# Performance work log

Hardware: AMD Instinct MI355X
Metric: run time of the kernel (lower is better)

Reference implementation:

```python
import jax, jax.numpy as jnp
import numpy as np

# ---- straight-through estimators (match torch floor_ste/round_ste in I-ViT) ----
def ste_floor(x):
    return x + jax.lax.stop_gradient(jnp.floor(x) - x)

def ste_round(x):
    return x + jax.lax.stop_gradient(jnp.round(x) - x)

# ---- QuantAct: symmetric per-tensor activation quantization ----
def quant_act(x, bit):
    qmax = 2.0 ** (bit - 1) - 1
    s = jnp.max(jnp.abs(jax.lax.stop_gradient(x))) / qmax
    x_int = jnp.clip(ste_round(x / s), -qmax - 1.0, qmax)
    return x_int * s, s

# ---- QuantLinear: per-output-channel symmetric weight quant, integer GEMM ----
def quant_linear(x, s_x, W, b=None, bit=8):
    qmax = 2.0 ** (bit - 1) - 1
    w_s = jnp.max(jnp.abs(jax.lax.stop_gradient(W)), axis=1, keepdims=True) / qmax  # [out,1]
    W_int = jnp.clip(ste_round(W / w_s), -qmax - 1.0, qmax)
    x_int = x / s_x                                   # [B,N,in] integer-valued
    out_s = w_s[:, 0] * s_x                           # [out] per-channel scale
    out_int = jnp.einsum('bni,oi->bno', x_int, W_int)
    if b is not None:
        out_int = out_int + ste_round(b / out_s)
    return out_int * out_s, out_s

# ---- IntSoftmax (I-ViT shift-based integer exp, output_bit=16) ----
def int_softmax(x, s, output_bit=16, n=15):
    x_int = x / s
    x_int = x_int - jnp.max(x_int, axis=-1, keepdims=True)
    # int_exp_shift: x*log2(e) approx via x + x/2 - x/16
    x_int = x_int + ste_floor(x_int / 2.0) - ste_floor(x_int / 16.0)
    x0 = jnp.floor(-1.0 / jax.lax.stop_gradient(s))   # floor(-1/s), negative
    x_int = jnp.maximum(x_int, n * x0)
    q = ste_floor(x_int / x0)                         # in [0, n]
    r = x_int - x0 * q
    exp_int = r / 2.0 - x0
    exp_int = jnp.clip(ste_floor(exp_int * jnp.exp2(n - q)), 0.0, None)
    exp_sum = jnp.minimum(jnp.sum(exp_int, axis=-1, keepdims=True), 2.0 ** 31 - 1)
    factor = ste_floor((2.0 ** 31 - 1) / exp_sum)
    exp_int = ste_floor(exp_int * factor / 2.0 ** (31 - output_bit + 1))
    out_s = jnp.asarray(1.0 / 2.0 ** (output_bit - 1), x.dtype)
    return exp_int * out_s, out_s

NUM_HEADS = 12

def attention_forward(x, s_in, W_qkv, W_proj, b_proj):
    B, N, C = x.shape
    H = NUM_HEADS
    D = C // H
    scale = D ** -0.5
    s_in = s_in.reshape(())
    # qkv QuantLinear (no bias) -> QuantAct(8)
    h, _ = quant_linear(x, s_in, W_qkv, None)
    h, s1 = quant_act(h, 8)
    qkv = h.reshape(B, N, 3, H, D).transpose(2, 0, 3, 1, 4)  # [3,B,H,N,D]
    q, k, v = qkv[0], qkv[1], qkv[2]
    # QuantMatMul 1: integer q @ k^T, rescale
    attn = jnp.einsum('bhnd,bhmd->bhnm', q / s1, k / s1) * (s1 * s1)
    s_attn = s1 * s1
    attn = attn * scale
    s_attn = s_attn * scale
    attn, s_attn = quant_act(attn, 8)
    attn, s_sm = int_softmax(attn, s_attn, output_bit=16)
    # QuantMatMul 2: integer attn @ v, rescale
    out = jnp.einsum('bhnm,bhmd->bhnd', attn / s_sm, v / s1) * (s_sm * s1)
    out = out.transpose(0, 2, 1, 3).reshape(B, N, C)
    out, s_o = quant_act(out, 8)
    out, _ = quant_linear(out, s_o, W_proj, b_proj)
    out, s_out = quant_act(out, 16)
    return out, s_out

def setup_inputs() -> dict:
    key = jax.random.key(0)
    k1, k2, k3, k4 = jax.random.split(key, 4)
    B, N, C = 8, 784, 768
    x = jax.random.normal(k1, (B, N, C), dtype=jnp.float32)
    # pre-quantize x so it is an integer multiple of its scaling factor (8-bit)
    s = jnp.max(jnp.abs(x)) / 127.0
    x = jnp.round(x / s) * s
    W_qkv = jax.random.normal(k2, (3 * C, C), dtype=jnp.float32) * (C ** -0.5)
    W_proj = jax.random.normal(k3, (C, C), dtype=jnp.float32) * (C ** -0.5)
    b_proj = jax.random.normal(k4, (C,), dtype=jnp.float32) * 0.02
    return {"x": x, "act_scaling_factor": s.reshape(1), "W_qkv": W_qkv,
            "W_proj": W_proj, "b_proj": b_proj}

def reference(x, act_scaling_factor, W_qkv, W_proj, b_proj):
    return attention_forward(x, act_scaling_factor, W_qkv, W_proj, b_proj)
```

## Files before the change

### kernel.cpp

```cpp
#include <hip/hip_runtime.h>
#include <cstdint>
#include <cstddef>

#define DEV __device__ __forceinline__

namespace {

constexpr int kN = 784, kC = 768, kH = 12, kD = 64;
constexpr int kM = 6272, kOC = 2304, kBH = 96;
constexpr int kNp = 832;
constexpr size_t SZ_QKV1 = (size_t)kBH * kN * kD;
constexpr size_t SZ_VT   = (size_t)kBH * kD * kNp;
constexpr double kEps   = 2.0e-3;
constexpr double kEpsW  = 3.0e-5;
constexpr double kEpsX0 = 3.0e-5;
constexpr long long kDS = 1024;
constexpr long long kEP = 128;
constexpr double kGuard = 1.0e-9;

using i32x4 = __attribute__((ext_vector_type(4))) int;

DEV void mfma_i8_acc(i32x4& c, i32x4 a, i32x4 b) {
  c = __builtin_amdgcn_mfma_i32_16x16x64_i8(a, b, c, 0, 0, 0);
}

DEV double wave_max_d(double v) {
  for (int o = 32; o; o >>= 1) v = fmax(v, __shfl_xor(v, o));
  return v;
}
DEV int wave_max_i(int v) {
  for (int o = 32; o; o >>= 1) v = max(v, __shfl_xor(v, o));
  return v;
}

DEV double ctl_hmax(const char* c)  { return __longlong_as_double(*(const long long*)(c)); }
DEV int    ctl_qkmax(const char* c) { return *(const int*)(c + 8); }
DEV double ctl_pmax(const char* c)  { return __longlong_as_double(*(const long long*)(c + 16)); }
DEV double ctl_pvmax(const char* c) { return __longlong_as_double(*(const long long*)(c + 24)); }

DEV double get_s1(const char* c) { return ctl_hmax(c) / 127.0; }
DEV double get_sa(const char* c) {
  double s1 = get_s1(c);
  double amax = ((double)ctl_qkmax(c) * (s1 * s1)) * 0.125;
  return amax / 127.0;
}
DEV double get_c2(const char* c) { return get_s1(c) * 3.0517578125e-05; }
DEV double get_so(const char* c) { return (ctl_pvmax(c) * get_c2(c)) / 127.0; }

DEV int p_eval(int xi, int x0i) {
  int x2 = xi + (xi >> 1) - (xi >> 4);
  x2 = max(x2, 15 * x0i);
  int q = x2 / x0i;
  int rrem = x2 - x0i * q;
  int base = rrem - 2 * x0i;
  return (q <= 14) ? (base << (14 - q)) : (base >> 1);
}

DEV int p4_final(long long p, long long fLo, long long fHi) {
  long long a = (p * fLo - kEP) >> 16;
  long long b = (p * fLo + kEP) >> 16;
  if (fLo == fHi) return (int)((a + b) << 1);
  long long c = (p * fHi - kEP) >> 16;
  long long d = (p * fHi + kEP) >> 16;
  return (int)(a + b + c + d);
}

__global__ __launch_bounds__(256) void k_quant_w(
    const float* __restrict__ Wq, const float* __restrict__ Wp,
    const float* __restrict__ s_in_p,
    int8_t* __restrict__ wq8A, int8_t* __restrict__ wq8B,
    int8_t* __restrict__ wp8A, int8_t* __restrict__ wp8B,
    double* __restrict__ outs_q, double* __restrict__ wsp) {
  int r = blockIdx.x;
  bool isq = r < kOC;
  const float* row = isq ? Wq + (size_t)r * kC : Wp + (size_t)(r - kOC) * kC;
  double m = 0.0;
  for (int i = threadIdx.x; i < kC; i += 256) m = fmax(m, fabs((double)row[i]));
  m = wave_max_d(m);
  __shared__ double sred[4];
  __shared__ double s_ws;
  if ((threadIdx.x & 63) == 0) sred[threadIdx.x >> 6] = m;
  __syncthreads();
  if (threadIdx.x == 0) {
    double mm = fmax(fmax(sred[0], sred[1]), fmax(sred[2], sred[3]));
    double ws = mm / 127.0;
    s_ws = ws;
    if (isq) outs_q[r] = ws * (double)s_in_p[0];
    else     wsp[r - kOC] = ws;
  }
  __syncthreads();
  double ws = s_ws;
  int8_t* dA = isq ? wq8A + (size_t)r * kC : wp8A + (size_t)(r - kOC) * kC;
  int8_t* dB = isq ? wq8B + (size_t)r * kC : wp8B + (size_t)(r - kOC) * kC;
  for (int i = threadIdx.x; i < kC; i += 256) {
    double arg = (double)row[i] / ws;
    dA[i] = (int8_t)(int)fmin(fmax(rint(arg - kEpsW), -128.0), 127.0);
    dB[i] = (int8_t)(int)fmin(fmax(rint(arg + kEpsW), -128.0), 127.0);
  }
}

__global__ __launch_bounds__(256) void k_quant_x(
    const float* __restrict__ x, const float* __restrict__ s_in_p,
    int8_t* __restrict__ x8) {
  double s = (double)s_in_p[0];
  int total = kM * kC;
  for (int i = blockIdx.x * 256 + threadIdx.x; i < total; i += gridDim.x * 256)
    x8[i] = (int8_t)(int)rint((double)x[i] / s);
}

template <int MODE>
__global__ __launch_bounds__(256) void k_gemm1m(
    const int8_t* __restrict__ A, const int8_t* __restrict__ Bm,
    const double* __restrict__ outs_q, char* __restrict__ ctl,
    int8_t* __restrict__ qkv8, int8_t* __restrict__ vT8, double dit) {
  __shared__ __align__(16) int8_t As[128][80];
  __shared__ __align__(16) int8_t Bs[128][80];
  int bm = blockIdx.y * 128, bn = blockIdx.x * 128;
  int tid = threadIdx.x;
  int w = tid >> 6, l = tid & 63;
  int frow = l & 15, fk = (l >> 4) << 4;
  int rb = w * 32;
  i32x4 acc[2][8];
#pragma unroll
  for (int i = 0; i < 2; ++i)
#pragma unroll
    for (int s = 0; s < 8; ++s) { acc[i][s][0]=0; acc[i][s][1]=0; acc[i][s][2]=0; acc[i][s][3]=0; }
  for (int k0 = 0; k0 < kC; k0 += 64) {
    __syncthreads();
#pragma unroll
    for (int e = 0; e < 2; ++e) {
      int idx = tid + e * 256;
      int row = idx >> 2, cg = (idx & 3) << 4;
      *(int4*)&As[row][cg] = *(const int4*)&A[(size_t)(bm + row) * kC + k0 + cg];
      *(int4*)&Bs[row][cg] = *(const int4*)&Bm[(size_t)(bn + row) * kC + k0 + cg];
    }
    __syncthreads();
    i32x4 af0 = *(const i32x4*)&As[rb + frow][fk];
    i32x4 af1 = *(const i32x4*)&As[rb + 16 + frow][fk];
#pragma unroll
    for (int s = 0; s < 8; ++s) {
      i32x4 bf = *(const i32x4*)&Bs[s * 16 + frow][fk];
      mfma_i8_acc(acc[0][s], af0, bf);
      mfma_i8_acc(acc[1][s], af1, bf);
    }
  }
  if (MODE == 0) {
    double m = 0.0;
#pragma unroll
    for (int s = 0; s < 8; ++s) {
      double oq = outs_q[bn + s * 16 + frow];
#pragma unroll
      for (int i = 0; i < 2; ++i)
#pragma unroll
        for (int r = 0; r < 4; ++r)
          m = fmax(m, fabs((double)acc[i][s][r] * oq));
    }
    m = wave_max_d(m);
    __shared__ double sred[4];
    if (l == 0) sred[w] = m;
    __syncthreads();
    if (tid == 0) {
      double mm = fmax(fmax(sred[0], sred[1]), fmax(sred[2], sred[3]));
      atomicMax((unsigned long long*)ctl,
                (unsigned long long)__double_as_longlong(mm));
    }
  } else {
    double s1 = get_s1(ctl);
    double inv_s1 = 1.0 / s1;
#pragma unroll
    for (int s = 0; s < 8; ++s) {
      int o = bn + s * 16 + frow;
      double oq = outs_q[o];
      int which = o / kC, rem = o % kC;
      int hh = rem >> 6, dd = rem & 63;
#pragma unroll
      for (int i = 0; i < 2; ++i)
#pragma unroll
        for (int r = 0; r < 4; ++r) {
          int n = bm + rb + i * 16 + ((l >> 4) << 2) + r;
          double num = (double)acc[i][s][r] * oq;
          double t = num * inv_s1 + dit;
          double r0 = rint(t);
          if (0.5 - fabs(t - r0) < kGuard) {
            t = num / s1 + dit;
            r0 = rint(t);
          }
          double v = fmin(fmax(r0, -128.0), 127.0);
          int bb = n / kN, nn = n % kN;
          int8_t q8v = (int8_t)(int)v;
          qkv8[(size_t)which * SZ_QKV1 + (((size_t)bb * kH + hh) * kN + nn) * kD + dd] = q8v;
          if (which == 2)
            vT8[((size_t)(bb * kH + hh) * kD + dd) * kNp + nn] = q8v;
        }
    }
  }
}

__global__ __launch_bounds__(256) void k_gemm_i8m(
    const int8_t* __restrict__ A, const int8_t* __restrict__ Bm,
    int* __restrict__ Cout, int Ncols, int K) {
  __shared__ __align__(16) int8_t As[128][80];
  __shared__ __align__(16) int8_t Bs[128][80];
  int bm = blockIdx.y * 128, bn = blockIdx.x * 128;
  int tid = threadIdx.x;
  int w = tid >> 6, l = tid & 63;
  int frow = l & 15, fk = (l >> 4) << 4;
  int rb = w * 32;
  i32x4 acc[2][8];
#pragma unroll
  for (int i = 0; i < 2; ++i)
#pragma unroll
    for (int s = 0; s < 8; ++s) { acc[i][s][0]=0; acc[i][s][1]=0; acc[i][s][2]=0; acc[i][s][3]=0; }
  for (int k0 = 0; k0 < K; k0 += 64) {
    __syncthreads();
#pragma unroll
    for (int e = 0; e < 2; ++e) {
      int idx = tid + e * 256;
      int row = idx >> 2, cg = (idx & 3) << 4;
      *(int4*)&As[row][cg] = *(const int4*)&A[(size_t)(bm + row) * K + k0 + cg];
      *(int4*)&Bs[row][cg] = *(const int4*)&Bm[(size_t)(bn + row) * K + k0 + cg];
    }
    __syncthreads();
    i32x4 af0 = *(const i32x4*)&As[rb + frow][fk];
    i32x4 af1 = *(const i32x4*)&As[rb + 16 + frow][fk];
#pragma unroll
    for (int s = 0; s < 8; ++s) {
      i32x4 bf = *(const i32x4*)&Bs[s * 16 + frow][fk];
      mfma_i8_acc(acc[0][s], af0, bf);
      mfma_i8_acc(acc[1][s], af1, bf);
    }
  }
#pragma unroll
  for (int s = 0; s < 8; ++s) {
    int n = bn + s * 16 + frow;
#pragma unroll
    for (int i = 0; i < 2; ++i)
#pragma unroll
      for (int r = 0; r < 4; ++r) {
        int m = bm + rb + i * 16 + ((l >> 4) << 2) + r;
        Cout[(size_t)m * Ncols + n] = acc[i][s][r];
      }
  }
}

__global__ __launch_bounds__(256) void k_qkmax2(
    const int8_t* __restrict__ qkv8, char* __restrict__ ctl) {
  int bh = blockIdx.x;
  const int8_t* qb = qkv8 + (size_t)bh * kN * kD;
  const int8_t* kb = qkv8 + SZ_QKV1 + (size_t)bh * kN * kD;
  __shared__ __align__(16) int8_t KS[784][80];
  int tid = threadIdx.x;
  for (int idx = tid; idx < 3136; idx += 256) {
    int row = idx >> 2, c16 = (idx & 3) << 4;
    *(int4*)&KS[row][c16] = *(const int4*)&kb[(size_t)row * kD + c16];
  }
  __syncthreads();
  int w = tid >> 6, l = tid & 63;
  int frow = l & 15, fk = (l >> 4) << 4;
  int mx = 0;
  for (int nt = w; nt < 49; nt += 4) {
    i32x4 af = *(const i32x4*)&qb[(size_t)(nt * 16 + frow) * kD + fk];
#pragma unroll 7
    for (int mt = 0; mt < 49; ++mt) {
      i32x4 bf = *(const i32x4*)&KS[mt * 16 + frow][fk];
      i32x4 c; c[0] = 0; c[1] = 0; c[2] = 0; c[3] = 0;
      mfma_i8_acc(c, af, bf);
      mx = max(mx, max(max(abs(c[0]), abs(c[1])), max(abs(c[2]), abs(c[3]))));
    }
  }
  mx = wave_max_i(mx);
  __shared__ int sred[4];
  if (l == 0) sred[w] = mx;
  __syncthreads();
  if (tid == 0) {
    int mm = max(max(sred[0], sred[1]), max(sred[2], sred[3]));
    atomicMax((int*)(ctl + 8), mm);
  }
}

__global__ __launch_bounds__(256) void k_attn(
    const int8_t* __restrict__ q8, const int8_t* __restrict__ k8,
    const int8_t* __restrict__ vT8, char* __restrict__ ctl,
    float* __restrict__ pv, double dit, double x0dit) {
  double s1 = get_s1(ctl);
  double s1s1 = s1 * s1;
  double s_a = get_sa(ctl);
  double inv_sa = 1.0 / s_a;
  double x0 = floor(-1.0 / s_a + x0dit);

  int bh = blockIdx.y;
  int n0 = blockIdx.x * 16;
  int bb = bh / kH, hh = bh % kH;
  const int8_t* kb = k8 + (size_t)bh * kN * kD;

  __shared__ __align__(16) int8_t Qs[16][64];
  __shared__ __align__(16) int8_t PL[3][16][848];

  int tid = threadIdx.x;
  int w = tid >> 6, l = tid & 63;

  {
    int row = tid >> 4, c4 = (tid & 15) << 2;
    *(int*)&Qs[row][c4] =
        *(const int*)&q8[((size_t)bh * kN + n0 + row) * kD + c4];
  }
  __syncthreads();

  {
    int frow = l & 15, fk = (l >> 4) << 4;
    i32x4 af = *(const i32x4*)&Qs[frow][fk];
    for (int t = w; t < 49; t += 4) {
      int m0 = t * 16;
      i32x4 bf = *(const i32x4*)&kb[(size_t)(m0 + frow) * kD + fk];
      i32x4 c; c[0] = 0; c[1] = 0; c[2] = 0; c[3] = 0;
      mfma_i8_acc(c, af, bf);
#pragma unroll
      for (int r = 0; r < 4; ++r) {
        int q = ((l >> 4) << 2) + r;
        double attnv = ((double)c[r] * s1s1) * 0.125;
        double t_f = attnv * inv_sa + dit;
        double r0 = rint(t_f);
        if (0.5 - fabs(t_f - r0) < kGuard) {
          double t_e = attnv / s_a + dit;
          r0 = rint(t_e);
        }
        double aq = fmin(fmax(r0, -128.0), 127.0);
        PL[0][q][m0 + frow] = (int8_t)(int)aq;
      }
    }
  }
  __syncthreads();

  {
    int x0i = (int)x0;
    int lane = l;
    for (int rr = 0; rr < 4; ++rr) {
      int row = w * 4 + rr;
      int rmax = -128;
#pragma unroll
      for (int i = 0; i < 13; ++i) {
        int m = lane + i * 64;
        if (m < kN) rmax = max(rmax, (int)(int8_t)PL[0][row][m]);
      }
      rmax = wave_max_i(rmax);
      int parr[13];
      long long sd = 0;
#pragma unroll
      for (int i = 0; i < 13; ++i) {
        int m = lane + i * 64;
        int p = 0;
        if (m < kN) { p = p_eval((int)(int8_t)PL[0][row][m] - rmax, x0i); sd += p; }
        parr[i] = p;
      }
      for (int off = 32; off; off >>= 1) sd += __shfl_xor(sd, off);
      long long S = sd > 2147483647LL ? 2147483647LL : sd;
      long long SLo = S + kDS;
      long long SHi = S - kDS; if (SHi < 1) SHi = 1;
      if (SLo > 2147483647LL) SLo = 2147483647LL;
      long long fLo = (long long)(2147483647u / (unsigned)SLo);
      long long fHi = (long long)(2147483647u / (unsigned)SHi);
#pragma unroll
      for (int i = 0; i < 13; ++i) {
        int m = lane + i * 64;
        if (m < kN) {
          int p4 = p4_final((long long)parr[i], fLo, fHi);
          int b0 = (int)(int8_t)(p4 & 0xff);
          int t1 = (p4 - b0) >> 8;
          int b1 = (int)(int8_t)(t1 & 0xff);
          int b2 = (t1 - b1) >> 8;
          PL[0][row][m] = (int8_t)b0;
          PL[1][row][m] = (int8_t)b1;
          PL[2][row][m] = (int8_t)b2;
        }
      }
      for (int m = kN + lane; m < 832; m += 64) {
        PL[0][row][m] = 0; PL[1][row][m] = 0; PL[2][row][m] = 0;
      }
    }
  }
  __syncthreads();

  {
    int frow = l & 15;
    int fk = (l >> 4) << 4;
    int dglob = w * 16 + frow;
    const int8_t* vtb = vT8 + ((size_t)bh * kD + dglob) * kNp;
    i32x4 a0, a1, a2;
    a0[0]=0;a0[1]=0;a0[2]=0;a0[3]=0;
    a1[0]=0;a1[1]=0;a1[2]=0;a1[3]=0;
    a2[0]=0;a2[1]=0;a2[2]=0;a2[3]=0;
    for (int mt = 0; mt < 13; ++mt) {
      int m0 = mt * 64;
      i32x4 bf = *(const i32x4*)&vtb[m0 + fk];
      i32x4 f0 = *(const i32x4*)&PL[0][frow][m0 + fk];
      i32x4 f1 = *(const i32x4*)&PL[1][frow][m0 + fk];
      i32x4 f2 = *(const i32x4*)&PL[2][frow][m0 + fk];
      mfma_i8_acc(a0, f0, bf);
      mfma_i8_acc(a1, f1, bf);
      mfma_i8_acc(a2, f2, bf);
    }
    double mymax = 0.0;
    int qhi = l >> 4;
#pragma unroll
    for (int r = 0; r < 4; ++r) {
      int q = qhi * 4 + r;
      long long tot = (long long)a0[r] + ((long long)a1[r] << 8) +
                      ((long long)a2[r] << 16);
      double v = 0.25 * (double)tot;
      pv[((size_t)bb * kN + (n0 + q)) * kC + hh * kD + dglob] = (float)v;
      mymax = fmax(mymax, fabs(v));
    }
    mymax = wave_max_d(mymax);
    __shared__ double sredd[4];
    if (l == 0) sredd[w] = mymax;
    __syncthreads();
    if (tid == 0) {
      double mm = fmax(fmax(sredd[0], sredd[1]), fmax(sredd[2], sredd[3]));
      atomicMax((unsigned long long*)(ctl + 24),
                (unsigned long long)__double_as_longlong(mm));
    }
  }
}

__global__ __launch_bounds__(256) void k_prep(
    const double* __restrict__ wsp, const float* __restrict__ bias,
    const char* __restrict__ ctl, double* __restrict__ outsv,
    double* __restrict__ bintA, double* __restrict__ bintB) {
  double s_o = get_so(ctl);
  int o = blockIdx.x * 256 + threadIdx.x;
  if (o < kC) {
    double outs = wsp[o] * s_o;
    outsv[o] = outs;
    double base = (double)bias[o] / outs;
    bintA[o] = rint(base - kEps);
    bintB[o] = rint(base + kEps);
  }
}

__global__ __launch_bounds__(256) void k_quant_o(
    const float* __restrict__ pv, const char* __restrict__ ctl,
    int8_t* __restrict__ o8, double dit) {
  double c2 = get_c2(ctl);
  double s_o = get_so(ctl);
  int total = kM * kC;
  for (int i = blockIdx.x * 256 + threadIdx.x; i < total; i += gridDim.x * 256) {
    double arg = ((double)pv[i] * c2) / s_o;
    double v = fmin(fmax(rint(arg + dit), -128.0), 127.0);
    o8[i] = (int8_t)(int)v;
  }
}

__global__ __launch_bounds__(256) void k_bias_max(
    int* __restrict__ p2, const double* __restrict__ outsv,
    const double* __restrict__ bint, char* __restrict__ ctl) {
  int n = blockIdx.x;
  int* rowp = p2 + (size_t)n * kC;
  double m = 0.0;
  for (int o = threadIdx.x; o < kC; o += 256) {
    int a = rowp[o] + (int)bint[o];
    rowp[o] = a;
    m = fmax(m, fabs((double)a * outsv[o]));
  }
  m = wave_max_d(m);
  __shared__ double sred[4];
  if ((threadIdx.x & 63) == 0) sred[threadIdx.x >> 6] = m;
  __syncthreads();
  if (threadIdx.x == 0) {
    double mm = fmax(fmax(sred[0], sred[1]), fmax(sred[2], sred[3]));
    atomicMax((unsigned long long*)(ctl + 16),
              (unsigned long long)__double_as_longlong(mm));
  }
}

__global__ __launch_bounds__(256) void k_final(
    const int* __restrict__ p2A, const int* __restrict__ p2B,
    const double* __restrict__ outsv,
    const char* __restrict__ ctl, float* __restrict__ out) {
  double s_out = ctl_pmax(ctl) / 32767.0;
  int total = kM * kC;
  for (int i = blockIdx.x * 256 + threadIdx.x; i < total; i += gridDim.x * 256) {
    int o = i % kC;
    double outs = outsv[o];
    double vA = fmin(fmax(rint(((double)p2A[i] * outs) / s_out - kEps), -32768.0), 32767.0);
    double vB = fmin(fmax(rint(((double)p2B[i] * outs) / s_out + kEps), -32768.0), 32767.0);
    out[i] = (float)(0.5 * (vA + vB) * s_out);
  }
  if (blockIdx.x == 0 && threadIdx.x == 0) out[total] = (float)s_out;
}

}

extern "C" void kernel_launch(void* const* d_in, const int* in_sizes, int n_in,
                              void* d_out, int out_size, void* d_ws, size_t ws_size,
                              hipStream_t stream) {
  const float* x   = (const float*)d_in[0];
  const float* sin = (const float*)d_in[1];
  const float* Wq  = (const float*)d_in[2];
  const float* Wp  = (const float*)d_in[3];
  const float* bp  = (const float*)d_in[4];
  float* out = (float*)d_out;

  char* ws = (char*)d_ws;
  char* ctl = ws;
  size_t off = 1024;
  int8_t* x8   = (int8_t*)(ws + off); off += (size_t)kM * kC;
  int8_t* wq8A = (int8_t*)(ws + off); off += (size_t)kOC * kC;
  int8_t* wq8B = (int8_t*)(ws + off); off += (size_t)kOC * kC;
  int8_t* wp8A = (int8_t*)(ws + off); off += (size_t)kC * kC;
  int8_t* wp8B = (int8_t*)(ws + off); off += (size_t)kC * kC;
  off = (off + 255) & ~(size_t)255;
  double* outs_q = (double*)(ws + off); off += (size_t)kOC * 8;
  double* wsp    = (double*)(ws + off); off += (size_t)kC * 8;
  double* outsv  = (double*)(ws + off); off += (size_t)kC * 8;
  double* bintA  = (double*)(ws + off); off += (size_t)kC * 8;
  double* bintB  = (double*)(ws + off); off += (size_t)kC * 8;
  off = (off + 255) & ~(size_t)255;
  int8_t* qkvA = (int8_t*)(ws + off); off += 3 * SZ_QKV1;
  int8_t* qkvB = (int8_t*)(ws + off); off += 3 * SZ_QKV1;
  int8_t* qA = qkvA, *kA = qkvA + SZ_QKV1;
  int8_t* qB = qkvB, *kB = qkvB + SZ_QKV1;
  off = (off + 255) & ~(size_t)255;
  int8_t* vT8A = (int8_t*)(ws + off); off += SZ_VT;
  int8_t* vT8B = (int8_t*)(ws + off); off += SZ_VT;
  int8_t* o8A = (int8_t*)(ws + off); off += (size_t)kM * kC;
  int8_t* o8B = (int8_t*)(ws + off); off += (size_t)kM * kC;
  off = (off + 255) & ~(size_t)255;
  float* pvA = (float*)(ws + off); int* p2A = (int*)pvA; off += (size_t)kM * kC * 4;
  float* pvB = (float*)(ws + off); int* p2B = (int*)pvB; off += (size_t)kM * kC * 4;

  dim3 g1(kOC / 128, kM / 128);
  hipMemsetAsync(ctl, 0, 1024, stream);
  k_quant_w<<<kOC + kC, 256, 0, stream>>>(Wq, Wp, sin, wq8A, wq8B, wp8A, wp8B,
                                          outs_q, wsp);
  k_quant_x<<<2048, 256, 0, stream>>>(x, sin, x8);
  k_gemm1m<0><<<g1, 256, 0, stream>>>(x8, wq8A, outs_q, ctl, nullptr, nullptr, 0.0);
  k_gemm1m<0><<<g1, 256, 0, stream>>>(x8, wq8B, outs_q, ctl, nullptr, nullptr, 0.0);
  k_gemm1m<1><<<g1, 256, 0, stream>>>(x8, wq8A, outs_q, ctl, qkvA, vT8A, -kEps);
  k_gemm1m<1><<<g1, 256, 0, stream>>>(x8, wq8B, outs_q, ctl, qkvB, vT8B, +kEps);
  k_qkmax2<<<kBH, 256, 0, stream>>>(qkvA, ctl);
  k_qkmax2<<<kBH, 256, 0, stream>>>(qkvB, ctl);
  k_attn<<<dim3(49, kBH), 256, 0, stream>>>(qA, kA, vT8A, ctl, pvA, -kEps, -kEpsX0);
  k_attn<<<dim3(49, kBH), 256, 0, stream>>>(qB, kB, vT8B, ctl, pvB, +kEps, +kEpsX0);
  k_prep<<<3, 256, 0, stream>>>(wsp, bp, ctl, outsv, bintA, bintB);
  k_quant_o<<<2048, 256, 0, stream>>>(pvA, ctl, o8A, -kEps);
  k_quant_o<<<2048, 256, 0, stream>>>(pvB, ctl, o8B, +kEps);
  k_gemm_i8m<<<dim3(kC / 128, kM / 128), 256, 0, stream>>>(o8A, wp8A, p2A, kC, kC);
  k_gemm_i8m<<<dim3(kC / 128, kM / 128), 256, 0, stream>>>(o8B, wp8B, p2B, kC, kC);
  k_bias_max<<<kM, 256, 0, stream>>>(p2A, outsv, bintA, ctl);
  k_bias_max<<<kM, 256, 0, stream>>>(p2B, outsv, bintB, ctl);
  k_final<<<2048, 256, 0, stream>>>(p2A, p2B, outsv, ctl, out);
}
```

Measured before the change: 797.0 us.

## Compute QKV GEMM once and patch B variant with sparse weight-flip corrections

Instead of running the QKV int8 GEMM four times (max pass and quantize pass for both A and B weight roundings), the GEMM runs once on the A weights and stores int32 results. The few weights that round differently in B are recorded as flips, and a sparse per-column correction is accumulated from x8 and applied when quantizing the B path, with a separate column-max pass. The softmax integer division is replaced by a magic-multiply, and reciprocal multiplication with a tie-guard fallback is added in the attention and output quant. This adds a large int32 intermediate buffer, extra memsets and atomic-heavy correction kernels, and the flip and column caps could truncate corrections if exceeded.

```diff
diff --git a/kernel.cpp b/kernel.cpp
--- a/kernel.cpp
+++ b/kernel.cpp
@@ -9,6 +9,8 @@
 constexpr int kN = 784, kC = 768, kH = 12, kD = 64;
 constexpr int kM = 6272, kOC = 2304, kBH = 96;
 constexpr int kNp = 832;
+constexpr int kMaxFlips = 4096;
+constexpr int kMaxUCols = 512;
 constexpr size_t SZ_QKV1 = (size_t)kBH * kN * kD;
 constexpr size_t SZ_VT   = (size_t)kBH * kD * kNp;
 constexpr double kEps   = 2.0e-3;
@@ -47,10 +49,11 @@
 DEV double get_c2(const char* c) { return get_s1(c) * 3.0517578125e-05; }
 DEV double get_so(const char* c) { return (ctl_pvmax(c) * get_c2(c)) / 127.0; }
 
-DEV int p_eval(int xi, int x0i) {
+DEV int p_eval_m(int xi, int x0i, int m15, unsigned long long magicM) {
   int x2 = xi + (xi >> 1) - (xi >> 4);
-  x2 = max(x2, 15 * x0i);
-  int q = x2 / x0i;
+  x2 = max(x2, m15);
+  unsigned long long n = (unsigned long long)(unsigned)(-x2);
+  int q = (int)((n * magicM) >> 32);
   int rrem = x2 - x0i * q;
   int base = rrem - 2 * x0i;
   return (q <= 14) ? (base << (14 - q)) : (base >> 1);
@@ -70,7 +73,8 @@
     const float* __restrict__ s_in_p,
     int8_t* __restrict__ wq8A, int8_t* __restrict__ wq8B,
     int8_t* __restrict__ wp8A, int8_t* __restrict__ wp8B,
-    double* __restrict__ outs_q, double* __restrict__ wsp) {
+    double* __restrict__ outs_q, double* __restrict__ wsp,
+    char* __restrict__ ctl, int4* __restrict__ flips) {
   int r = blockIdx.x;
   bool isq = r < kOC;
   const float* row = isq ? Wq + (size_t)r * kC : Wp + (size_t)(r - kOC) * kC;
@@ -94,8 +98,14 @@
   int8_t* dB = isq ? wq8B + (size_t)r * kC : wp8B + (size_t)(r - kOC) * kC;
   for (int i = threadIdx.x; i < kC; i += 256) {
     double arg = (double)row[i] / ws;
-    dA[i] = (int8_t)(int)fmin(fmax(rint(arg - kEpsW), -128.0), 127.0);
-    dB[i] = (int8_t)(int)fmin(fmax(rint(arg + kEpsW), -128.0), 127.0);
+    int vA = (int)fmin(fmax(rint(arg - kEpsW), -128.0), 127.0);
+    int vB = (int)fmin(fmax(rint(arg + kEpsW), -128.0), 127.0);
+    dA[i] = (int8_t)vA;
+    dB[i] = (int8_t)vB;
+    if (isq && vA != vB) {
+      int idx = atomicAdd((int*)(ctl + 12), 1);
+      if (idx < kMaxFlips) flips[idx] = make_int4(r, i, vB - vA, 0);
+    }
   }
 }
 
@@ -108,11 +118,10 @@
     x8[i] = (int8_t)(int)rint((double)x[i] / s);
 }
 
-template <int MODE>
-__global__ __launch_bounds__(256) void k_gemm1m(
+__global__ __launch_bounds__(256) void k_gemm1c(
     const int8_t* __restrict__ A, const int8_t* __restrict__ Bm,
     const double* __restrict__ outs_q, char* __restrict__ ctl,
-    int8_t* __restrict__ qkv8, int8_t* __restrict__ vT8, double dit) {
+    int* __restrict__ C1) {
   __shared__ __align__(16) int8_t As[128][80];
   __shared__ __align__(16) int8_t Bs[128][80];
   int bm = blockIdx.y * 128, bn = blockIdx.x * 128;
@@ -144,55 +153,113 @@
       mfma_i8_acc(acc[1][s], af1, bf);
     }
   }
-  if (MODE == 0) {
-    double m = 0.0;
-#pragma unroll
-    for (int s = 0; s < 8; ++s) {
-      double oq = outs_q[bn + s * 16 + frow];
-#pragma unroll
-      for (int i = 0; i < 2; ++i)
-#pragma unroll
-        for (int r = 0; r < 4; ++r)
-          m = fmax(m, fabs((double)acc[i][s][r] * oq));
-    }
-    m = wave_max_d(m);
-    __shared__ double sred[4];
-    if (l == 0) sred[w] = m;
-    __syncthreads();
-    if (tid == 0) {
-      double mm = fmax(fmax(sred[0], sred[1]), fmax(sred[2], sred[3]));
-      atomicMax((unsigned long long*)ctl,
-                (unsigned long long)__double_as_longlong(mm));
-    }
-  } else {
-    double s1 = get_s1(ctl);
-    double inv_s1 = 1.0 / s1;
-#pragma unroll
-    for (int s = 0; s < 8; ++s) {
-      int o = bn + s * 16 + frow;
-      double oq = outs_q[o];
-      int which = o / kC, rem = o % kC;
-      int hh = rem >> 6, dd = rem & 63;
-#pragma unroll
-      for (int i = 0; i < 2; ++i)
-#pragma unroll
-        for (int r = 0; r < 4; ++r) {
-          int n = bm + rb + i * 16 + ((l >> 4) << 2) + r;
-          double num = (double)acc[i][s][r] * oq;
-          double t = num * inv_s1 + dit;
-          double r0 = rint(t);
-          if (0.5 - fabs(t - r0) < kGuard) {
-            t = num / s1 + dit;
-            r0 = rint(t);
-          }
-          double v = fmin(fmax(r0, -128.0), 127.0);
-          int bb = n / kN, nn = n % kN;
-          int8_t q8v = (int8_t)(int)v;
-          qkv8[(size_t)which * SZ_QKV1 + (((size_t)bb * kH + hh) * kN + nn) * kD + dd] = q8v;
-          if (which == 2)
-            vT8[((size_t)(bb * kH + hh) * kD + dd) * kNp + nn] = q8v;
-        }
-    }
+  double m = 0.0;
+#pragma unroll
+  for (int s = 0; s < 8; ++s) {
+    int o = bn + s * 16 + frow;
+    double oq = outs_q[o];
+#pragma unroll
+    for (int i = 0; i < 2; ++i)
+#pragma unroll
+      for (int r = 0; r < 4; ++r) {
+        int n = bm + rb + i * 16 + ((l >> 4) << 2) + r;
+        int v = acc[i][s][r];
+        C1[(size_t)n * kOC + o] = v;
+        m = fmax(m, fabs((double)v * oq));
+      }
+  }
+  m = wave_max_d(m);
+  __shared__ double sred[4];
+  if (l == 0) sred[w] = m;
+  __syncthreads();
+  if (tid == 0) {
+    double mm = fmax(fmax(sred[0], sred[1]), fmax(sred[2], sred[3]));
+    atomicMax((unsigned long long*)ctl,
+              (unsigned long long)__double_as_longlong(mm));
+  }
+}
+
+__global__ void k_colmap(char* __restrict__ ctl, const int4* __restrict__ flips,
+                         short* __restrict__ colmap, int* __restrict__ ucol) {
+  if (threadIdx.x != 0 || blockIdx.x != 0) return;
+  int cnt = min(*(const int*)(ctl + 12), kMaxFlips);
+  int u = 0;
+  for (int f = 0; f < cnt; ++f) {
+    int o = flips[f].x;
+    if (colmap[o] < 0 && u < kMaxUCols) { colmap[o] = (short)u; ucol[u] = o; ++u; }
+  }
+  *(int*)(ctl + 32) = u;
+}
+
+__global__ __launch_bounds__(256) void k_colfix(
+    const char* __restrict__ ctl, const int4* __restrict__ flips,
+    const short* __restrict__ colmap, const int8_t* __restrict__ x8,
+    int* __restrict__ Ccorr) {
+  int cnt = min(*(const int*)(ctl + 12), kMaxFlips);
+  for (int f = blockIdx.x; f < cnt; f += gridDim.x) {
+    int o = flips[f].x, i = flips[f].y, d = flips[f].z;
+    int u = colmap[o];
+    if (u < 0) continue;
+    for (int n = threadIdx.x; n < kM; n += 256)
+      atomicAdd(&Ccorr[(size_t)n * kMaxUCols + u], d * (int)x8[(size_t)n * kC + i]);
+  }
+}
+
+__global__ __launch_bounds__(256) void k_colmax(
+    char* __restrict__ ctl, const int* __restrict__ ucol,
+    const int* __restrict__ C1, const int* __restrict__ Ccorr,
+    const double* __restrict__ outs_q) {
+  int u = blockIdx.x;
+  if (u >= *(const int*)(ctl + 32)) return;
+  int o = ucol[u];
+  double oq = outs_q[o];
+  double m = 0.0;
+  for (int n = threadIdx.x; n < kM; n += 256) {
+    int c = C1[(size_t)n * kOC + o] + Ccorr[(size_t)n * kMaxUCols + u];
+    m = fmax(m, fabs((double)c * oq));
+  }
+  m = wave_max_d(m);
+  __shared__ double sred[4];
+  if ((threadIdx.x & 63) == 0) sred[threadIdx.x >> 6] = m;
+  __syncthreads();
+  if (threadIdx.x == 0) {
+    double mm = fmax(fmax(sred[0], sred[1]), fmax(sred[2], sred[3]));
+    atomicMax((unsigned long long*)ctl,
+              (unsigned long long)__double_as_longlong(mm));
+  }
+}
+
+template <int BR>
+__global__ __launch_bounds__(256) void k_quant_h(
+    const int* __restrict__ C1, const int* __restrict__ Ccorr,
+    const short* __restrict__ colmap, const double* __restrict__ outs_q,
+    const char* __restrict__ ctl, int8_t* __restrict__ qkv8,
+    int8_t* __restrict__ vT8, double dit) {
+  double s1 = get_s1(ctl);
+  double inv_s1 = 1.0 / s1;
+  int total = kM * kOC;
+  for (int i = blockIdx.x * 256 + threadIdx.x; i < total; i += gridDim.x * 256) {
+    int n = i / kOC, o = i - n * kOC;
+    int c = C1[i];
+    if (BR) {
+      int u = colmap[o];
+      if (u >= 0) c += Ccorr[(size_t)n * kMaxUCols + u];
+    }
+    double num = (double)c * outs_q[o];
+    double t = num * inv_s1 + dit;
+    double r0 = rint(t);
+    if (0.5 - fabs(t - r0) < kGuard) {
+      t = num / s1 + dit;
+      r0 = rint(t);
+    }
+    double v = fmin(fmax(r0, -128.0), 127.0);
+    int which = o / kC, rem = o - which * kC;
+    int hh = rem >> 6, dd = rem & 63;
+    int bb = n / kN, nn = n - bb * kN;
+    int8_t q8v = (int8_t)(int)v;
+    qkv8[(size_t)which * SZ_QKV1 + (((size_t)bb * kH + hh) * kN + nn) * kD + dd] = q8v;
+    if (which == 2)
+      vT8[((size_t)(bb * kH + hh) * kD + dd) * kNp + nn] = q8v;
   }
 }
 
@@ -286,7 +353,13 @@
   double s1s1 = s1 * s1;
   double s_a = get_sa(ctl);
   double inv_sa = 1.0 / s_a;
+  double cfast = (s1s1 * 0.125) * inv_sa;
   double x0 = floor(-1.0 / s_a + x0dit);
+  int x0i = (int)x0;
+  int dpos = -x0i;
+  unsigned long long magicM =
+      (0x100000000ULL + (unsigned long long)(dpos - 1)) / (unsigned long long)dpos;
+  int m15 = 15 * x0i;
 
   int bh = blockIdx.y;
   int n0 = blockIdx.x * 16;
@@ -317,12 +390,11 @@
 #pragma unroll
       for (int r = 0; r < 4; ++r) {
         int q = ((l >> 4) << 2) + r;
-        double attnv = ((double)c[r] * s1s1) * 0.125;
-        double t_f = attnv * inv_sa + dit;
+        double t_f = (double)c[r] * cfast + dit;
         double r0 = rint(t_f);
         if (0.5 - fabs(t_f - r0) < kGuard) {
-          double t_e = attnv / s_a + dit;
-          r0 = rint(t_e);
+          double attnv = ((double)c[r] * s1s1) * 0.125;
+          r0 = rint(attnv / s_a + dit);
         }
         double aq = fmin(fmax(r0, -128.0), 127.0);
         PL[0][q][m0 + frow] = (int8_t)(int)aq;
@@ -332,7 +404,6 @@
   __syncthreads();
 
   {
-    int x0i = (int)x0;
     int lane = l;
     for (int rr = 0; rr < 4; ++rr) {
       int row = w * 4 + rr;
@@ -349,7 +420,10 @@
       for (int i = 0; i < 13; ++i) {
         int m = lane + i * 64;
         int p = 0;
-        if (m < kN) { p = p_eval((int)(int8_t)PL[0][row][m] - rmax, x0i); sd += p; }
+        if (m < kN) {
+          p = p_eval_m((int)(int8_t)PL[0][row][m] - rmax, x0i, m15, magicM);
+          sd += p;
+        }
         parr[i] = p;
       }
       for (int off = 32; off; off >>= 1) sd += __shfl_xor(sd, off);
@@ -442,10 +516,14 @@
     int8_t* __restrict__ o8, double dit) {
   double c2 = get_c2(ctl);
   double s_o = get_so(ctl);
+  double inv_so = 1.0 / s_o;
   int total = kM * kC;
   for (int i = blockIdx.x * 256 + threadIdx.x; i < total; i += gridDim.x * 256) {
-    double arg = ((double)pv[i] * c2) / s_o;
-    double v = fmin(fmax(rint(arg + dit), -128.0), 127.0);
+    double num = (double)pv[i] * c2;
+    double t = num * inv_so + dit;
+    double r0 = rint(t);
+    if (0.5 - fabs(t - r0) < kGuard) r0 = rint(num / s_o + dit);
+    double v = fmin(fmax(r0, -128.0), 127.0);
     o8[i] = (int8_t)(int)v;
   }
 }
@@ -503,6 +581,11 @@
   char* ws = (char*)d_ws;
   char* ctl = ws;
   size_t off = 1024;
+  int4*  flips  = (int4*)(ws + off);  off += (size_t)kMaxFlips * 16;
+  short* colmap = (short*)(ws + off); off += (size_t)kOC * 2;
+  off = (off + 255) & ~(size_t)255;
+  int*   ucol   = (int*)(ws + off);   off += (size_t)kMaxUCols * 4;
+  off = (off + 255) & ~(size_t)255;
   int8_t* x8   = (int8_t*)(ws + off); off += (size_t)kM * kC;
   int8_t* wq8A = (int8_t*)(ws + off); off += (size_t)kOC * kC;
   int8_t* wq8B = (int8_t*)(ws + off); off += (size_t)kOC * kC;
@@ -525,18 +608,27 @@
   int8_t* o8A = (int8_t*)(ws + off); off += (size_t)kM * kC;
   int8_t* o8B = (int8_t*)(ws + off); off += (size_t)kM * kC;
   off = (off + 255) & ~(size_t)255;
-  float* pvA = (float*)(ws + off); int* p2A = (int*)pvA; off += (size_t)kM * kC * 4;
-  float* pvB = (float*)(ws + off); int* p2B = (int*)pvB; off += (size_t)kM * kC * 4;
+  int* Ccorr = (int*)(ws + off); off += (size_t)kM * kMaxUCols * 4;
+  off = (off + 255) & ~(size_t)255;
+  int* C1A = (int*)(ws + off); off += (size_t)kM * kOC * 4;
+  float* pvA = (float*)C1A;                 int* p2A = (int*)pvA;
+  float* pvB = (float*)((char*)C1A + (size_t)kM * kC * 4); int* p2B = (int*)pvB;
 
   dim3 g1(kOC / 128, kM / 128);
   hipMemsetAsync(ctl, 0, 1024, stream);
+  hipMemsetAsync(colmap, 0xFF, (size_t)kOC * 2, stream);
+  hipMemsetAsync(Ccorr, 0, (size_t)kM * kMaxUCols * 4, stream);
   k_quant_w<<<kOC + kC, 256, 0, stream>>>(Wq, Wp, sin, wq8A, wq8B, wp8A, wp8B,
-                                          outs_q, wsp);
+                                          outs_q, wsp, ctl, flips);
   k_quant_x<<<2048, 256, 0, stream>>>(x, sin, x8);
-  k_gemm1m<0><<<g1, 256, 0, stream>>>(x8, wq8A, outs_q, ctl, nullptr, nullptr, 0.0);
-  k_gemm1m<0><<<g1, 256, 0, stream>>>(x8, wq8B, outs_q, ctl, nullptr, nullptr, 0.0);
-  k_gemm1m<1><<<g1, 256, 0, stream>>>(x8, wq8A, outs_q, ctl, qkvA, vT8A, -kEps);
-  k_gemm1m<1><<<g1, 256, 0, stream>>>(x8, wq8B, outs_q, ctl, qkvB, vT8B, +kEps);
+  k_gemm1c<<<g1, 256, 0, stream>>>(x8, wq8A, outs_q, ctl, C1A);
+  k_colmap<<<1, 64, 0, stream>>>(ctl, flips, colmap, ucol);
+  k_colfix<<<256, 256, 0, stream>>>(ctl, flips, colmap, x8, Ccorr);
+  k_colmax<<<kMaxUCols, 256, 0, stream>>>(ctl, ucol, C1A, Ccorr, outs_q);
+  k_quant_h<0><<<2048, 256, 0, stream>>>(C1A, Ccorr, colmap, outs_q, ctl,
+                                         qkvA, vT8A, -kEps);
+  k_quant_h<1><<<2048, 256, 0, stream>>>(C1A, Ccorr, colmap, outs_q, ctl,
+                                         qkvB, vT8B, +kEps);
   k_qkmax2<<<kBH, 256, 0, stream>>>(qkvA, ctl);
   k_qkmax2<<<kBH, 256, 0, stream>>>(qkvB, ctl);
   k_attn<<<dim3(49, kBH), 256, 0, stream>>>(qA, kA, vT8A, ctl, pvA, -kEps, -kEpsX0);
```

Result: no change. 805.9 us (+1.1%).
